# Performance work log

Hardware: AMD Instinct MI355X
Metric: run time of the kernel (lower is better)

The kernel has to match this reference:

```python
import jax, jax.numpy as jnp
import numpy as np

PI = np.pi
NQ = 9  # qubits: edge 0-2, node 3-6 (center=3, neighbor0=4), anc1=7, anc2=8


def _mlp(x, W1, b1, W2, b2):
    h = jax.nn.leaky_relu(x @ W1 + b1, negative_slope=0.2)
    return h @ W2 + b2


def _ry(t):
    h = 0.5 * t
    c = jnp.cos(h).astype(jnp.complex64)
    s = jnp.sin(h).astype(jnp.complex64)
    return jnp.stack([jnp.stack([c, -s]), jnp.stack([s, c])])


def _rx(t):
    h = 0.5 * t
    c = jnp.cos(h).astype(jnp.complex64)
    s = jnp.sin(h).astype(jnp.complex64)
    return jnp.stack([jnp.stack([c, -1j * s]), jnp.stack([-1j * s, c])])


def _rz(t):
    h = (0.5 * t).astype(jnp.complex64)
    e = jnp.exp(-1j * h)
    z = jnp.zeros((), jnp.complex64)
    return jnp.stack([jnp.stack([e, z]), jnp.stack([z, jnp.conj(e)])])


def _ap1(state, U, q):
    s = jnp.moveaxis(state, q, 0)
    s = jnp.tensordot(U, s, axes=([1], [0]))
    return jnp.moveaxis(s, 0, q)


def _apc(state, U, c, t):  # controlled-U, control c, target t
    s = jnp.moveaxis(state, (c, t), (0, 1))
    s1 = jnp.tensordot(U, s[1], axes=([1], [0]))
    s = jnp.stack([s[0], s1])
    return jnp.moveaxis(s, (0, 1), (c, t))


def _cz(state, a, b):
    s = jnp.moveaxis(state, (a, b), (0, 1))
    s = s.at[1, 1].multiply(-1.0)
    return jnp.moveaxis(s, (0, 1), (a, b))


def _pqc(data, theta):
    # data: [18] per-graphlet angles, theta: [27] shared weights; returns <X_center>
    state = jnp.zeros((2,) * NQ, jnp.complex64).at[(0,) * NQ].set(1.0)
    for i in range(3):  # edge qubits: ry, rz
        state = _ap1(state, _ry(data[2 * i]), i)
        state = _ap1(state, _rz(data[2 * i + 1]), i)
    for i in range(4):  # node qubits: ry, rz
        state = _ap1(state, _ry(data[6 + 2 * i]), 3 + i)
        state = _ap1(state, _rz(data[7 + 2 * i]), 3 + i)
    state = _apc(state, _rx(data[14]), 4, 7)  # neighbor -> anc1, c-rx(phi0)
    state = _apc(state, _ry(data[15]), 0, 7)  # edge0    -> anc1, c-ry(phi1)
    state = _apc(state, _rz(data[16]), 4, 8)  # neighbor -> anc2, c-rz(phi2)
    state = _apc(state, _ry(data[17]), 0, 8)  # edge0    -> anc2, c-ry(phi3)
    for b, qs in enumerate([(0, 4, 7), (7, 4, 8), (3, 7, 8)]):  # A, B, U blocks
        th = theta[9 * b:9 * b + 9]
        for i, q in enumerate(qs):
            state = _ap1(state, _rx(th[3 * i + 0]), q)
            state = _ap1(state, _ry(th[3 * i + 1]), q)
            state = _ap1(state, _rz(th[3 * i + 2]), q)
        state = _cz(state, qs[0], qs[1])
        state = _cz(state, qs[1], qs[2])
        state = _cz(state, qs[2], qs[0])
    xs = jnp.moveaxis(jnp.moveaxis(state, 3, 0)[::-1], 0, 3)  # apply X on qubit 3
    return jnp.real(jnp.vdot(state, xs)).astype(jnp.float32)


def setup_inputs() -> dict:
    N, E, K, G = 6000, 96000, 4, 32
    rng = np.random.default_rng(0)
    src = rng.integers(0, N, E)
    dst = (src + 1 + rng.integers(0, N - 1, E)) % N  # no self loops
    pairs = np.stack([np.minimum(src, dst), np.maximum(src, dst)], 1)
    keymap = {(int(u), int(v)): i for i, (u, v) in enumerate(pairs)}
    und = np.unique(np.concatenate([np.stack([src, dst], 1), np.stack([dst, src], 1)], 0), axis=0)
    deg = np.bincount(und[:, 0], minlength=N)
    starts = np.concatenate([[0], np.cumsum(deg)])[:-1]
    gn = np.full((N, K), -1, np.int32)
    gn[:, 0] = np.arange(N)
    ge = np.full((N, K - 1), -1, np.int32)
    for j in range(K - 1):
        has = deg > j
        cs = np.nonzero(has)[0]
        nb = und[starts[has] + j, 1]
        gn[cs, 1 + j] = nb
        for c, n in zip(cs.tolist(), nb.tolist()):
            ge[c, j] = keymap[(min(c, n), max(c, n))]
    batch = ((np.arange(N) * G) // N).astype(np.int32)
    key = jax.random.key(0)
    ks = jax.random.split(key, 12)

    def dense(k, i, o):
        return jax.random.normal(k, (i, o), jnp.float32) / np.sqrt(i)

    return dict(
        node_feat=jax.random.normal(ks[0], (N, 16), jnp.float32),
        edge_attr=jax.random.normal(ks[1], (E, 8), jnp.float32),
        node_W1=dense(ks[2], 16, 128), node_b1=jnp.zeros((128,), jnp.float32),
        node_W2=dense(ks[3], 128, 2), node_b2=jnp.zeros((2,), jnp.float32),
        edge_W1=dense(ks[4], 8, 128), edge_b1=jnp.zeros((128,), jnp.float32),
        edge_W2=dense(ks[5], 128, 2), edge_b2=jnp.zeros((2,), jnp.float32),
        theta=jax.random.uniform(ks[6], (1, 27), jnp.float32, -0.1, 0.1),
        upd_W1=dense(ks[7], 3, 128)[None], upd_b1=jnp.zeros((1, 128), jnp.float32),
        upd_W2=dense(ks[8], 128, 2)[None], upd_b2=jnp.zeros((1, 2), jnp.float32),
        head_W1=dense(ks[9], 2, 2), head_b1=jnp.zeros((2,), jnp.float32),
        head_W2=dense(ks[10], 2, 2), head_b2=jnp.zeros((2,), jnp.float32),
        graphlet_nodes=jnp.asarray(gn), graphlet_edges=jnp.asarray(ge),
        batch=jnp.asarray(batch), num_graphs=G,
    )


def reference(node_feat, edge_attr, node_W1, node_b1, node_W2, node_b2,
              edge_W1, edge_b1, edge_W2, edge_b2, theta,
              upd_W1, upd_b1, upd_W2, upd_b2,
              head_W1, head_b1, head_W2, head_b2,
              graphlet_nodes, graphlet_edges, batch, num_graphs):
    node_f = jnp.tanh(_mlp(node_feat, node_W1, node_b1, node_W2, node_b2)) * PI
    edge_f = jnp.tanh(_mlp(edge_attr, edge_W1, edge_b1, edge_W2, edge_b2)) * PI
    nm = (graphlet_nodes >= 0).astype(node_f.dtype)[..., None]  # pad mask
    em = (graphlet_edges >= 0).astype(edge_f.dtype)[..., None]
    gn = jnp.clip(graphlet_nodes, 0)
    ge = jnp.clip(graphlet_edges, 0)
    N = node_f.shape[0]
    e_feat = edge_f[ge] * em  # [N,3,2] fixed across hops
    for h in range(theta.shape[0]):
        n_feat = node_f[gn] * nm  # [N,4,2]
        phis = jnp.stack([n_feat[:, 1, 0], e_feat[:, 0, 0], n_feat[:, 1, 1], e_feat[:, 0, 1]], 1)
        data = jnp.concatenate([e_feat.reshape(N, 6), n_feat.reshape(N, 8), phis], 1)  # [N,18]
        exp = jax.vmap(_pqc, in_axes=(0, None))(data, theta[h])  # [N]
        upd_inp = jnp.concatenate([node_f[gn[:, 0]], exp[:, None]], 1)  # [N,3]
        upd = _mlp(upd_inp, upd_W1[h], upd_b1[h], upd_W2[h], upd_b2[h])  # [N,2]
        node_f = node_f + jnp.zeros_like(node_f).at[gn[:, 0]].add(upd)
    seg = jax.ops.segment_sum(node_f, batch, num_segments=num_graphs)
    cnt = jax.ops.segment_sum(jnp.ones((N,), node_f.dtype), batch, num_segments=num_graphs)
    emb = seg / cnt[:, None]  # global mean pool
    return _mlp(emb, head_W1, head_b1, head_W2, head_b2)
```

## Files before the change

kernel.cpp:

```cpp
#include <hip/hip_runtime.h>

#define PI_F 3.14159265358979323846f

struct C2 { float r, i; };
struct M2 { C2 m[2][2]; };

__device__ __forceinline__ C2 cmul(C2 a, C2 b){ return C2{a.r*b.r - a.i*b.i, a.r*b.i + a.i*b.r}; }
__device__ __forceinline__ C2 cadd(C2 a, C2 b){ return C2{a.r+b.r, a.i+b.i}; }

__device__ __forceinline__ M2 mmul(M2 A, M2 B){
  M2 R;
  #pragma unroll
  for (int r=0;r<2;++r)
    #pragma unroll
    for (int c=0;c<2;++c)
      R.m[r][c] = cadd(cmul(A.m[r][0],B.m[0][c]), cmul(A.m[r][1],B.m[1][c]));
  return R;
}
__device__ __forceinline__ M2 m_rx(float t){ float s,c; __sincosf(0.5f*t,&s,&c);
  M2 U; U.m[0][0]=C2{c,0}; U.m[0][1]=C2{0,-s}; U.m[1][0]=C2{0,-s}; U.m[1][1]=C2{c,0}; return U; }
__device__ __forceinline__ M2 m_ry(float t){ float s,c; __sincosf(0.5f*t,&s,&c);
  M2 U; U.m[0][0]=C2{c,0}; U.m[0][1]=C2{-s,0}; U.m[1][0]=C2{s,0}; U.m[1][1]=C2{c,0}; return U; }
__device__ __forceinline__ M2 m_rz(float t){ float s,c; __sincosf(0.5f*t,&s,&c);
  M2 U; U.m[0][0]=C2{c,-s}; U.m[0][1]=C2{0,0}; U.m[1][0]=C2{0,0}; U.m[1][1]=C2{c,s}; return U; }
__device__ __forceinline__ M2 fuse_zyx(float tz, float ty, float tx){ return mmul(m_rz(tz), mmul(m_ry(ty), m_rx(tx))); }

__device__ __forceinline__ float fast_tanh(float x){
  float e = __expf(2.f*x);
  return 1.f - 2.f/(e + 1.f);
}

__device__ __forceinline__ M2 loadM(const float* __restrict__ p){
  M2 U;
  U.m[0][0]=C2{p[0],p[1]}; U.m[0][1]=C2{p[2],p[3]};
  U.m[1][0]=C2{p[4],p[5]}; U.m[1][1]=C2{p[6],p[7]};
  return U;
}


template<int T>
__device__ __forceinline__ void applyT(M2 U, float (&sr)[32], float (&si)[32]){
  #pragma unroll
  for (int a0=0;a0<32;++a0){
    if (a0 & T) continue;
    const int a1 = a0 | T;
    C2 x0{sr[a0], si[a0]}, x1{sr[a1], si[a1]};
    C2 n0 = cadd(cmul(U.m[0][0],x0), cmul(U.m[0][1],x1));
    C2 n1 = cadd(cmul(U.m[1][0],x0), cmul(U.m[1][1],x1));
    sr[a0]=n0.r; si[a0]=n0.i; sr[a1]=n1.r; si[a1]=n1.i;
  }
}

template<int BA,int BB,int BC>
__device__ __forceinline__ void czTriple(float (&sr)[32], float (&si)[32]){
  #pragma unroll
  for (int a=0;a<32;++a){
    const int x=(a&BA)?1:0, y=(a&BB)?1:0, z=(a&BC)?1:0;
    if (((x&y)^(y&z)^(z&x)) != 0){ sr[a]=-sr[a]; si[a]=-si[a]; }
  }
}

__global__ void features_kernel(const float* __restrict__ node_feat,
                                const float* __restrict__ edge_attr,
                                const int* __restrict__ ge,
                                const float* __restrict__ nW1, const float* __restrict__ nb1,
                                const float* __restrict__ nW2, const float* __restrict__ nb2,
                                const float* __restrict__ eW1, const float* __restrict__ eb1,
                                const float* __restrict__ eW2, const float* __restrict__ eb2,
                                float* __restrict__ node_f, float* __restrict__ ef,
                                int N,
                                const float* __restrict__ theta, float* __restrict__ tm){
  const int row = blockIdx.x*blockDim.x + threadIdx.x;
  if (row < 9){
    M2 U = fuse_zyx(theta[3*row+2], theta[3*row+1], theta[3*row+0]);
    float* p = tm + row*8;
    p[0]=U.m[0][0].r; p[1]=U.m[0][0].i;
    p[2]=U.m[0][1].r; p[3]=U.m[0][1].i;
    p[4]=U.m[1][0].r; p[5]=U.m[1][0].i;
    p[6]=U.m[1][1].r; p[7]=U.m[1][1].i;
  }
  if (row < N){
    float xi[16];
    #pragma unroll
    for (int i=0;i<16;++i) xi[i] = node_feat[row*16+i];
    float a0 = nb2[0], a1 = nb2[1];
    #pragma unroll 4
    for (int j=0;j<128;++j){
      float h = nb1[j];
      #pragma unroll
      for (int i=0;i<16;++i) h = fmaf(xi[i], nW1[i*128+j], h);
      h = h > 0.f ? h : 0.2f*h;
      a0 = fmaf(h, nW2[j*2+0], a0);
      a1 = fmaf(h, nW2[j*2+1], a1);
    }
    node_f[row*2+0] = PI_F * fast_tanh(a0);
    node_f[row*2+1] = PI_F * fast_tanh(a1);
  } else {
    const int r = row - N;
    if (r >= N) return;
    const int e = ge[r*3+0];
    if (e < 0){ ef[r*2+0] = 0.f; ef[r*2+1] = 0.f; return; }
    float xi[8];
    #pragma unroll
    for (int i=0;i<8;++i) xi[i] = edge_attr[e*8+i];
    float a0 = eb2[0], a1 = eb2[1];
    #pragma unroll 4
    for (int j=0;j<128;++j){
      float h = eb1[j];
      #pragma unroll
      for (int i=0;i<8;++i) h = fmaf(xi[i], eW1[i*128+j], h);
      h = h > 0.f ? h : 0.2f*h;
      a0 = fmaf(h, eW2[j*2+0], a0);
      a1 = fmaf(h, eW2[j*2+1], a1);
    }
    ef[r*2+0] = PI_F * fast_tanh(a0);
    ef[r*2+1] = PI_F * fast_tanh(a1);
  }
}

__global__ void __launch_bounds__(64, 1)
pqc_kernel(const float* __restrict__ node_f, const float* __restrict__ ef,
           const int* __restrict__ gn,
           const float* __restrict__ tm,
           const float* __restrict__ uW1, const float* __restrict__ ub1,
           const float* __restrict__ uW2, const float* __restrict__ ub2,
           float* __restrict__ upd, int N){
  const int n = blockIdx.x*64 + threadIdx.x;
  if (n >= N) return;

  const float e0 = ef[n*2+0], e1 = ef[n*2+1];
  const float f0 = node_f[n*2+0], f1 = node_f[n*2+1];
  const int v1 = gn[n*4+1];
  const bool ok = v1 >= 0; const int idx = ok ? v1 : 0;
  const float g0 = ok ? node_f[idx*2+0] : 0.f;
  const float g1 = ok ? node_f[idx*2+1] : 0.f;

  float sy0,cy0,sz0,cz0, sy3,cy3,sz3,cz3, sy4,cy4,sz4,cz4;
  __sincosf(0.5f*e0,&sy0,&cy0); __sincosf(0.5f*e1,&sz0,&cz0);
  __sincosf(0.5f*f0,&sy3,&cy3); __sincosf(0.5f*f1,&sz3,&cz3);
  __sincosf(0.5f*g0,&sy4,&cy4); __sincosf(0.5f*g1,&sz4,&cz4);

  const C2 v0[2] = { C2{cy0*cz0, -cy0*sz0}, C2{sy0*cz0, sy0*sz0} };
  const C2 v3[2] = { C2{cy3*cz3, -cy3*sz3}, C2{sy3*cz3, sy3*sz3} };
  const C2 v4[2] = { C2{cy4*cz4, -cy4*sz4}, C2{sy4*cz4, sy4*sz4} };

  float sr[32], si[32];
  #pragma unroll
  for (int a=0;a<32;++a){ sr[a]=0.f; si[a]=0.f; }
  #pragma unroll
  for (int b4=0;b4<2;++b4){
    #pragma unroll
    for (int b3=0;b3<2;++b3){
      const C2 t = cmul(v0[b4], v3[b3]);
      #pragma unroll
      for (int b2=0;b2<2;++b2){
        const C2 a = cmul(t, v4[b2]);
        const int ix = b4*16 + b3*8 + b2*4;
        sr[ix]=a.r; si[ix]=a.i;
      }
    }
  }

  #pragma unroll
  for (int a0=0;a0<32;++a0){
    if ((a0 & 2) || !(a0 & 4)) continue;
    const int a1 = a0 | 2;
    const float r0=sr[a0], i0=si[a0], r1=sr[a1], i1=si[a1];
    sr[a0] = cy4*r0 + sy4*i1;  si[a0] = cy4*i0 - sy4*r1;
    sr[a1] = sy4*i0 + cy4*r1;  si[a1] = -sy4*r0 + cy4*i1;
  }
  #pragma unroll
  for (int a0=0;a0<32;++a0){
    if ((a0 & 2) || !(a0 & 16)) continue;
    const int a1 = a0 | 2;
    const float r0=sr[a0], i0=si[a0], r1=sr[a1], i1=si[a1];
    sr[a0] = cy0*r0 - sy0*r1;  si[a0] = cy0*i0 - sy0*i1;
    sr[a1] = sy0*r0 + cy0*r1;  si[a1] = sy0*i0 + cy0*i1;
  }
  #pragma unroll
  for (int a=0;a<32;++a){
    if (!(a & 4)) continue;
    const float r=sr[a], im=si[a];
    if (a & 1){ sr[a] = r*cz4 - im*sz4;  si[a] = im*cz4 + r*sz4; }
    else      { sr[a] = r*cz4 + im*sz4;  si[a] = im*cz4 - r*sz4; }
  }
  #pragma unroll
  for (int a0=0;a0<32;++a0){
    if ((a0 & 1) || !(a0 & 16)) continue;
    const int a1 = a0 | 1;
    const float r0=sr[a0], i0=si[a0], r1=sr[a1], i1=si[a1];
    sr[a0] = cz0*r0 - sz0*r1;  si[a0] = cz0*i0 - sz0*i1;
    sr[a1] = sz0*r0 + cz0*r1;  si[a1] = sz0*i0 + cz0*i1;
  }

  applyT<16>(loadM(tm+0*8), sr, si);
  applyT< 4>(loadM(tm+1*8), sr, si);
  applyT< 2>(loadM(tm+2*8), sr, si);
  czTriple<16,4,2>(sr, si);
  applyT< 2>(loadM(tm+3*8), sr, si);
  applyT< 4>(loadM(tm+4*8), sr, si);
  applyT< 1>(loadM(tm+5*8), sr, si);
  czTriple<2,4,1>(sr, si);
  applyT< 8>(loadM(tm+6*8), sr, si);
  applyT< 2>(loadM(tm+7*8), sr, si);
  applyT< 1>(loadM(tm+8*8), sr, si);
  czTriple<8,2,1>(sr, si);

  float acc = 0.f;
  #pragma unroll
  for (int a=0;a<32;++a) acc += sr[a]*sr[a^8] + si[a]*si[a^8];

  float o0 = ub2[0], o1 = ub2[1];
  #pragma unroll 4
  for (int j=0;j<128;++j){
    float h = ub1[j];
    h = fmaf(f0,  uW1[0*128+j], h);
    h = fmaf(f1,  uW1[1*128+j], h);
    h = fmaf(acc, uW1[2*128+j], h);
    h = h > 0.f ? h : 0.2f*h;
    o0 = fmaf(h, uW2[j*2+0], o0);
    o1 = fmaf(h, uW2[j*2+1], o1);
  }
  upd[n*2+0] = o0;
  upd[n*2+1] = o1;
}

__global__ void reduce_head_kernel(const float* __restrict__ node_f,
                                   const float* __restrict__ upd,
                                   const float* __restrict__ hW1, const float* __restrict__ hb1,
                                   const float* __restrict__ hW2, const float* __restrict__ hb2,
                                   float* __restrict__ out, int N, int G){
  const int g = blockIdx.x;
  const int start = (g*N + G - 1)/G;
  const int end   = ((g+1)*N + G - 1)/G;
  float a0=0.f, a1=0.f;
  for (int n = start + threadIdx.x; n < end; n += 64){
    a0 += node_f[n*2+0] + upd[n*2+0];
    a1 += node_f[n*2+1] + upd[n*2+1];
  }
  #pragma unroll
  for (int m=32; m; m>>=1){ a0 += __shfl_xor(a0, m); a1 += __shfl_xor(a1, m); }
  if (threadIdx.x == 0){
    const float inv = 1.f / (float)(end - start);
    const float e0 = a0*inv, e1 = a1*inv;
    float h0 = hb1[0] + e0*hW1[0*2+0] + e1*hW1[1*2+0];
    float h1 = hb1[1] + e0*hW1[0*2+1] + e1*hW1[1*2+1];
    h0 = h0 > 0.f ? h0 : 0.2f*h0;
    h1 = h1 > 0.f ? h1 : 0.2f*h1;
    out[g*2+0] = hb2[0] + h0*hW2[0*2+0] + h1*hW2[1*2+0];
    out[g*2+1] = hb2[1] + h0*hW2[0*2+1] + h1*hW2[1*2+1];
  }
}

extern "C" void kernel_launch(void* const* d_in, const int* in_sizes, int n_in,
                              void* d_out, int out_size, void* d_ws, size_t ws_size,
                              hipStream_t stream) {
  const float* node_feat = (const float*)d_in[0];
  const float* edge_attr = (const float*)d_in[1];
  const float* nW1 = (const float*)d_in[2];
  const float* nb1 = (const float*)d_in[3];
  const float* nW2 = (const float*)d_in[4];
  const float* nb2 = (const float*)d_in[5];
  const float* eW1 = (const float*)d_in[6];
  const float* eb1 = (const float*)d_in[7];
  const float* eW2 = (const float*)d_in[8];
  const float* eb2 = (const float*)d_in[9];
  const float* theta = (const float*)d_in[10];
  const float* uW1 = (const float*)d_in[11];
  const float* ub1 = (const float*)d_in[12];
  const float* uW2 = (const float*)d_in[13];
  const float* ub2 = (const float*)d_in[14];
  const float* hW1 = (const float*)d_in[15];
  const float* hb1 = (const float*)d_in[16];
  const float* hW2 = (const float*)d_in[17];
  const float* hb2 = (const float*)d_in[18];
  const int* gn    = (const int*)d_in[19];
  const int* ge    = (const int*)d_in[20];

  const int N = in_sizes[0] / 16;
  const int G = out_size / 2;

  float* node_f = (float*)d_ws;
  float* ef     = node_f + (size_t)N*2;
  float* upd    = ef + (size_t)N*2;
  float* tm     = upd + (size_t)N*2;

  const int R = 2*N;
  features_kernel<<<(R+255)/256, 256, 0, stream>>>(node_feat, edge_attr, ge,
                                                   nW1, nb1, nW2, nb2,
                                                   eW1, eb1, eW2, eb2,
                                                   node_f, ef, N, theta, tm);
  pqc_kernel<<<(N+63)/64, 64, 0, stream>>>(node_f, ef, gn, tm,
                                           uW1, ub1, uW2, ub2, upd, N);
  reduce_head_kernel<<<G, 64, 0, stream>>>(node_f, upd,
                                           hW1, hb1, hW2, hb2, (float*)d_out, N, G);
}
```

Before: 141.2 us.

## Fuse pooling and head into PQC kernel via last-block atomic counter

Removes the separate reduce_head kernel launch by having the last block that finishes the PQC kernel perform the per-graph mean pool and head MLP, detected through an atomic completion counter reset in the features kernel. The PQC block size also grows from 64 to 256 threads. Updates are written with atomicExch and read back with agent-scope atomic loads so the last block sees them. The trade-off is one launch saved against a serialized tail where a single block reduces all graphs with only 4 waves, and fewer, larger blocks for the PQC work.

Result: slower. 148.0 us (+4.8%).

```diff
diff --git a/kernel.cpp b/kernel.cpp
--- a/kernel.cpp
+++ b/kernel.cpp
@@ -69,8 +69,10 @@
                                 const float* __restrict__ eW2, const float* __restrict__ eb2,
                                 float* __restrict__ node_f, float* __restrict__ ef,
                                 int N,
-                                const float* __restrict__ theta, float* __restrict__ tm){
+                                const float* __restrict__ theta, float* __restrict__ tm,
+                                unsigned int* __restrict__ done){
   const int row = blockIdx.x*blockDim.x + threadIdx.x;
+  if (row == 0) *done = 0u;
   if (row < 9){
     M2 U = fuse_zyx(theta[3*row+2], theta[3*row+1], theta[3*row+0]);
     float* p = tm + row*8;
@@ -118,137 +120,150 @@
   }
 }
 
-__global__ void __launch_bounds__(64, 1)
+__global__ void __launch_bounds__(256, 1)
 pqc_kernel(const float* __restrict__ node_f, const float* __restrict__ ef,
            const int* __restrict__ gn,
            const float* __restrict__ tm,
            const float* __restrict__ uW1, const float* __restrict__ ub1,
            const float* __restrict__ uW2, const float* __restrict__ ub2,
-           float* __restrict__ upd, int N){
-  const int n = blockIdx.x*64 + threadIdx.x;
-  if (n >= N) return;
-
-  const float e0 = ef[n*2+0], e1 = ef[n*2+1];
-  const float f0 = node_f[n*2+0], f1 = node_f[n*2+1];
-  const int v1 = gn[n*4+1];
-  const bool ok = v1 >= 0; const int idx = ok ? v1 : 0;
-  const float g0 = ok ? node_f[idx*2+0] : 0.f;
-  const float g1 = ok ? node_f[idx*2+1] : 0.f;
-
-  float sy0,cy0,sz0,cz0, sy3,cy3,sz3,cz3, sy4,cy4,sz4,cz4;
-  __sincosf(0.5f*e0,&sy0,&cy0); __sincosf(0.5f*e1,&sz0,&cz0);
-  __sincosf(0.5f*f0,&sy3,&cy3); __sincosf(0.5f*f1,&sz3,&cz3);
-  __sincosf(0.5f*g0,&sy4,&cy4); __sincosf(0.5f*g1,&sz4,&cz4);
-
-  const C2 v0[2] = { C2{cy0*cz0, -cy0*sz0}, C2{sy0*cz0, sy0*sz0} };
-  const C2 v3[2] = { C2{cy3*cz3, -cy3*sz3}, C2{sy3*cz3, sy3*sz3} };
-  const C2 v4[2] = { C2{cy4*cz4, -cy4*sz4}, C2{sy4*cz4, sy4*sz4} };
-
-  float sr[32], si[32];
-  #pragma unroll
-  for (int a=0;a<32;++a){ sr[a]=0.f; si[a]=0.f; }
-  #pragma unroll
-  for (int b4=0;b4<2;++b4){
-    #pragma unroll
-    for (int b3=0;b3<2;++b3){
-      const C2 t = cmul(v0[b4], v3[b3]);
+           const float* __restrict__ hW1, const float* __restrict__ hb1,
+           const float* __restrict__ hW2, const float* __restrict__ hb2,
+           float* upd, float* __restrict__ out,
+           unsigned int* done,
+           int N, int G){
+  const int n = blockIdx.x*256 + threadIdx.x;
+
+  if (n < N){
+    const float e0 = ef[n*2+0], e1 = ef[n*2+1];
+    const float f0 = node_f[n*2+0], f1 = node_f[n*2+1];
+    const int v1 = gn[n*4+1];
+    const bool ok = v1 >= 0; const int idx = ok ? v1 : 0;
+    const float g0 = ok ? node_f[idx*2+0] : 0.f;
+    const float g1 = ok ? node_f[idx*2+1] : 0.f;
+
+    float sy0,cy0,sz0,cz0, sy3,cy3,sz3,cz3, sy4,cy4,sz4,cz4;
+    __sincosf(0.5f*e0,&sy0,&cy0); __sincosf(0.5f*e1,&sz0,&cz0);
+    __sincosf(0.5f*f0,&sy3,&cy3); __sincosf(0.5f*f1,&sz3,&cz3);
+    __sincosf(0.5f*g0,&sy4,&cy4); __sincosf(0.5f*g1,&sz4,&cz4);
+
+    const C2 v0[2] = { C2{cy0*cz0, -cy0*sz0}, C2{sy0*cz0, sy0*sz0} };
+    const C2 v3[2] = { C2{cy3*cz3, -cy3*sz3}, C2{sy3*cz3, sy3*sz3} };
+    const C2 v4[2] = { C2{cy4*cz4, -cy4*sz4}, C2{sy4*cz4, sy4*sz4} };
+
+    float sr[32], si[32];
+    #pragma unroll
+    for (int a=0;a<32;++a){ sr[a]=0.f; si[a]=0.f; }
+    #pragma unroll
+    for (int b4=0;b4<2;++b4){
       #pragma unroll
-      for (int b2=0;b2<2;++b2){
-        const C2 a = cmul(t, v4[b2]);
-        const int ix = b4*16 + b3*8 + b2*4;
-        sr[ix]=a.r; si[ix]=a.i;
+      for (int b3=0;b3<2;++b3){
+        const C2 t = cmul(v0[b4], v3[b3]);
+        #pragma unroll
+        for (int b2=0;b2<2;++b2){
+          const C2 a = cmul(t, v4[b2]);
+          const int ix = b4*16 + b3*8 + b2*4;
+          sr[ix]=a.r; si[ix]=a.i;
+        }
       }
     }
-  }
-
-  #pragma unroll
-  for (int a0=0;a0<32;++a0){
-    if ((a0 & 2) || !(a0 & 4)) continue;
-    const int a1 = a0 | 2;
-    const float r0=sr[a0], i0=si[a0], r1=sr[a1], i1=si[a1];
-    sr[a0] = cy4*r0 + sy4*i1;  si[a0] = cy4*i0 - sy4*r1;
-    sr[a1] = sy4*i0 + cy4*r1;  si[a1] = -sy4*r0 + cy4*i1;
-  }
-  #pragma unroll
-  for (int a0=0;a0<32;++a0){
-    if ((a0 & 2) || !(a0 & 16)) continue;
-    const int a1 = a0 | 2;
-    const float r0=sr[a0], i0=si[a0], r1=sr[a1], i1=si[a1];
-    sr[a0] = cy0*r0 - sy0*r1;  si[a0] = cy0*i0 - sy0*i1;
-    sr[a1] = sy0*r0 + cy0*r1;  si[a1] = sy0*i0 + cy0*i1;
-  }
-  #pragma unroll
-  for (int a=0;a<32;++a){
-    if (!(a & 4)) continue;
-    const float r=sr[a], im=si[a];
-    if (a & 1){ sr[a] = r*cz4 - im*sz4;  si[a] = im*cz4 + r*sz4; }
-    else      { sr[a] = r*cz4 + im*sz4;  si[a] = im*cz4 - r*sz4; }
-  }
-  #pragma unroll
-  for (int a0=0;a0<32;++a0){
-    if ((a0 & 1) || !(a0 & 16)) continue;
-    const int a1 = a0 | 1;
-    const float r0=sr[a0], i0=si[a0], r1=sr[a1], i1=si[a1];
-    sr[a0] = cz0*r0 - sz0*r1;  si[a0] = cz0*i0 - sz0*i1;
-    sr[a1] = sz0*r0 + cz0*r1;  si[a1] = sz0*i0 + cz0*i1;
-  }
-
-  applyT<16>(loadM(tm+0*8), sr, si);
-  applyT< 4>(loadM(tm+1*8), sr, si);
-  applyT< 2>(loadM(tm+2*8), sr, si);
-  czTriple<16,4,2>(sr, si);
-  applyT< 2>(loadM(tm+3*8), sr, si);
-  applyT< 4>(loadM(tm+4*8), sr, si);
-  applyT< 1>(loadM(tm+5*8), sr, si);
-  czTriple<2,4,1>(sr, si);
-  applyT< 8>(loadM(tm+6*8), sr, si);
-  applyT< 2>(loadM(tm+7*8), sr, si);
-  applyT< 1>(loadM(tm+8*8), sr, si);
-  czTriple<8,2,1>(sr, si);
-
-  float acc = 0.f;
-  #pragma unroll
-  for (int a=0;a<32;++a) acc += sr[a]*sr[a^8] + si[a]*si[a^8];
-
-  float o0 = ub2[0], o1 = ub2[1];
-  #pragma unroll 4
-  for (int j=0;j<128;++j){
-    float h = ub1[j];
-    h = fmaf(f0,  uW1[0*128+j], h);
-    h = fmaf(f1,  uW1[1*128+j], h);
-    h = fmaf(acc, uW1[2*128+j], h);
-    h = h > 0.f ? h : 0.2f*h;
-    o0 = fmaf(h, uW2[j*2+0], o0);
-    o1 = fmaf(h, uW2[j*2+1], o1);
-  }
-  upd[n*2+0] = o0;
-  upd[n*2+1] = o1;
-}
-
-__global__ void reduce_head_kernel(const float* __restrict__ node_f,
-                                   const float* __restrict__ upd,
-                                   const float* __restrict__ hW1, const float* __restrict__ hb1,
-                                   const float* __restrict__ hW2, const float* __restrict__ hb2,
-                                   float* __restrict__ out, int N, int G){
-  const int g = blockIdx.x;
-  const int start = (g*N + G - 1)/G;
-  const int end   = ((g+1)*N + G - 1)/G;
-  float a0=0.f, a1=0.f;
-  for (int n = start + threadIdx.x; n < end; n += 64){
-    a0 += node_f[n*2+0] + upd[n*2+0];
-    a1 += node_f[n*2+1] + upd[n*2+1];
-  }
-  #pragma unroll
-  for (int m=32; m; m>>=1){ a0 += __shfl_xor(a0, m); a1 += __shfl_xor(a1, m); }
+
+    #pragma unroll
+    for (int a0=0;a0<32;++a0){
+      if ((a0 & 2) || !(a0 & 4)) continue;
+      const int a1 = a0 | 2;
+      const float r0=sr[a0], i0=si[a0], r1=sr[a1], i1=si[a1];
+      sr[a0] = cy4*r0 + sy4*i1;  si[a0] = cy4*i0 - sy4*r1;
+      sr[a1] = sy4*i0 + cy4*r1;  si[a1] = -sy4*r0 + cy4*i1;
+    }
+    #pragma unroll
+    for (int a0=0;a0<32;++a0){
+      if ((a0 & 2) || !(a0 & 16)) continue;
+      const int a1 = a0 | 2;
+      const float r0=sr[a0], i0=si[a0], r1=sr[a1], i1=si[a1];
+      sr[a0] = cy0*r0 - sy0*r1;  si[a0] = cy0*i0 - sy0*i1;
+      sr[a1] = sy0*r0 + cy0*r1;  si[a1] = sy0*i0 + cy0*i1;
+    }
+    #pragma unroll
+    for (int a=0;a<32;++a){
+      if (!(a & 4)) continue;
+      const float r=sr[a], im=si[a];
+      if (a & 1){ sr[a] = r*cz4 - im*sz4;  si[a] = im*cz4 + r*sz4; }
+      else      { sr[a] = r*cz4 + im*sz4;  si[a] = im*cz4 - r*sz4; }
+    }
+    #pragma unroll
+    for (int a0=0;a0<32;++a0){
+      if ((a0 & 1) || !(a0 & 16)) continue;
+      const int a1 = a0 | 1;
+      const float r0=sr[a0], i0=si[a0], r1=sr[a1], i1=si[a1];
+      sr[a0] = cz0*r0 - sz0*r1;  si[a0] = cz0*i0 - sz0*i1;
+      sr[a1] = sz0*r0 + cz0*r1;  si[a1] = sz0*i0 + cz0*i1;
+    }
+
+    applyT<16>(loadM(tm+0*8), sr, si);
+    applyT< 4>(loadM(tm+1*8), sr, si);
+    applyT< 2>(loadM(tm+2*8), sr, si);
+    czTriple<16,4,2>(sr, si);
+    applyT< 2>(loadM(tm+3*8), sr, si);
+    applyT< 4>(loadM(tm+4*8), sr, si);
+    applyT< 1>(loadM(tm+5*8), sr, si);
+    czTriple<2,4,1>(sr, si);
+    applyT< 8>(loadM(tm+6*8), sr, si);
+    applyT< 2>(loadM(tm+7*8), sr, si);
+    applyT< 1>(loadM(tm+8*8), sr, si);
+    czTriple<8,2,1>(sr, si);
+
+    float acc = 0.f;
+    #pragma unroll
+    for (int a=0;a<32;++a) acc += sr[a]*sr[a^8] + si[a]*si[a^8];
+
+    float o0 = ub2[0], o1 = ub2[1];
+    #pragma unroll 4
+    for (int j=0;j<128;++j){
+      float h = ub1[j];
+      h = fmaf(f0,  uW1[0*128+j], h);
+      h = fmaf(f1,  uW1[1*128+j], h);
+      h = fmaf(acc, uW1[2*128+j], h);
+      h = h > 0.f ? h : 0.2f*h;
+      o0 = fmaf(h, uW2[j*2+0], o0);
+      o1 = fmaf(h, uW2[j*2+1], o1);
+    }
+    atomicExch(&upd[n*2+0], o0);
+    atomicExch(&upd[n*2+1], o1);
+  }
+
+  __shared__ bool amLast;
+  __syncthreads();
   if (threadIdx.x == 0){
-    const float inv = 1.f / (float)(end - start);
-    const float e0 = a0*inv, e1 = a1*inv;
-    float h0 = hb1[0] + e0*hW1[0*2+0] + e1*hW1[1*2+0];
-    float h1 = hb1[1] + e0*hW1[0*2+1] + e1*hW1[1*2+1];
-    h0 = h0 > 0.f ? h0 : 0.2f*h0;
-    h1 = h1 > 0.f ? h1 : 0.2f*h1;
-    out[g*2+0] = hb2[0] + h0*hW2[0*2+0] + h1*hW2[1*2+0];
-    out[g*2+1] = hb2[1] + h0*hW2[0*2+1] + h1*hW2[1*2+1];
+    unsigned int old = atomicAdd(done, 1u);
+    amLast = (old == gridDim.x - 1);
+  }
+  __syncthreads();
+  if (!amLast) return;
+
+  const int lane = threadIdx.x & 63;
+  const int w = threadIdx.x >> 6;
+  for (int g = w; g < G; g += 4){
+    const int start = (g*N + G - 1)/G;
+    const int end   = ((g+1)*N + G - 1)/G;
+    float a0=0.f, a1=0.f;
+    for (int nn = start + lane; nn < end; nn += 64){
+      float u0 = __hip_atomic_load(&upd[nn*2+0], __ATOMIC_RELAXED, __HIP_MEMORY_SCOPE_AGENT);
+      float u1 = __hip_atomic_load(&upd[nn*2+1], __ATOMIC_RELAXED, __HIP_MEMORY_SCOPE_AGENT);
+      a0 += node_f[nn*2+0] + u0;
+      a1 += node_f[nn*2+1] + u1;
+    }
+    #pragma unroll
+    for (int m=32; m; m>>=1){ a0 += __shfl_xor(a0, m); a1 += __shfl_xor(a1, m); }
+    if (lane == 0){
+      const float inv = 1.f / (float)(end - start);
+      const float e0 = a0*inv, e1 = a1*inv;
+      float h0 = hb1[0] + e0*hW1[0*2+0] + e1*hW1[1*2+0];
+      float h1 = hb1[1] + e0*hW1[0*2+1] + e1*hW1[1*2+1];
+      h0 = h0 > 0.f ? h0 : 0.2f*h0;
+      h1 = h1 > 0.f ? h1 : 0.2f*h1;
+      out[g*2+0] = hb2[0] + h0*hW2[0*2+0] + h1*hW2[1*2+0];
+      out[g*2+1] = hb2[1] + h0*hW2[0*2+1] + h1*hW2[1*2+1];
+    }
   }
 }
 
@@ -284,14 +299,15 @@
   float* ef     = node_f + (size_t)N*2;
   float* upd    = ef + (size_t)N*2;
   float* tm     = upd + (size_t)N*2;
+  unsigned int* done = (unsigned int*)(tm + 80);
 
   const int R = 2*N;
   features_kernel<<<(R+255)/256, 256, 0, stream>>>(node_feat, edge_attr, ge,
                                                    nW1, nb1, nW2, nb2,
                                                    eW1, eb1, eW2, eb2,
-                                                   node_f, ef, N, theta, tm);
-  pqc_kernel<<<(N+63)/64, 64, 0, stream>>>(node_f, ef, gn, tm,
-                                           uW1, ub1, uW2, ub2, upd, N);
-  reduce_head_kernel<<<G, 64, 0, stream>>>(node_f, upd,
-                                           hW1, hb1, hW2, hb2, (float*)d_out, N, G);
-}
+                                                   node_f, ef, N, theta, tm, done);
+  pqc_kernel<<<(N+255)/256, 256, 0, stream>>>(node_f, ef, gn, tm,
+                                              uW1, ub1, uW2, ub2,
+                                              hW1, hb1, hW2, hb2,
+                                              upd, (float*)d_out, done, N, G);
+}
```
